# Optimization experiments

Measured on AMD Instinct MI355X. Metric: run time of the kernel, lower is better.

Reference implementation:

```python
import jax, jax.numpy as jnp
import numpy as np

T, B, D, H, R, O = 32, 8, 512, 512, 32, 512
CLIP_VAL = 1.0
LN_EPS = 1e-5


def setup_inputs() -> dict:
    key = jax.random.key(0)
    ks = jax.random.split(key, 8)
    rn = lambda k, sh, sc: (jax.random.normal(k, sh) * sc).astype(jnp.float32)
    inp = {
        'x': rn(ks[0], (T, B, D), 1.0),
        'h0': jnp.zeros((B, H), jnp.float32),
        'v0': jnp.zeros((B, H), jnp.float32),
        'dU0': jnp.zeros((B, H, H), jnp.float32),
        'trace_e0': jnp.zeros((B, H), jnp.float32),
        'trace_E0': jnp.zeros((B, H, H), jnp.float32),
        # parameters (init-scale approximations of the torch inits)
        'x2h_w': rn(ks[1], (2 * H, D), 1.0 / np.sqrt(D)),
        'x2h_b': jnp.zeros((2 * H,), jnp.float32),
        'h2h_w': rn(ks[2], (2 * H, H), 1.0 / np.sqrt(H)),
        'h2h_b': jnp.zeros((2 * H,), jnp.float32),
        'lnx_g': jnp.ones((2 * H,), jnp.float32),
        'lnx_b': jnp.zeros((2 * H,), jnp.float32),
        'lnh_g': jnp.ones((2 * H,), jnp.float32),
        'lnh_b': jnp.zeros((2 * H,), jnp.float32),
        'h2mod_w': rn(ks[3], (R, H), np.sqrt(2.0 / H)),
        'h2mod_b': jnp.zeros((R,), jnp.float32),
        'mod2h_w': rn(ks[4], (3, R), np.sqrt(2.0 / R)),
        'mod2h_b': jnp.zeros((3,), jnp.float32),
        'alpha': jnp.full((1,), -4.0, jnp.float32),
        'tau_U': jnp.full((1,), -4.5, jnp.float32),
        'dec_w': rn(ks[5], (O, H), 1.0 / np.sqrt(H)),
        'dec_b': jnp.zeros((O,), jnp.float32),
    }
    return inp


def _ln(y, g, b):
    mu = jnp.mean(y, axis=-1, keepdims=True)
    yc = y - mu
    var = jnp.mean(yc * yc, axis=-1, keepdims=True)
    return g * yc * jax.lax.rsqrt(var + LN_EPS) + b


def reference(x, h0, v0, dU0, trace_e0, trace_E0,
              x2h_w, x2h_b, h2h_w, h2h_b,
              lnx_g, lnx_b, lnh_g, lnh_b,
              h2mod_w, h2mod_b, mod2h_w, mod2h_b,
              alpha, tau_U, dec_w, dec_b):
    Hh = h0.shape[-1]
    sp_alpha = jax.nn.softplus(alpha)            # (1,)
    tau = jax.nn.sigmoid(tau_U)                  # (1,)
    # clip bounds derived from the candidate-row block of h2h weight
    w_dv = h2h_w[Hh:2 * Hh]                      # [H, H]
    upper = jax.nn.relu(CLIP_VAL - w_dv) / (sp_alpha + 1e-8)
    lower = -jax.nn.relu(CLIP_VAL + w_dv) / (sp_alpha + 1e-8)

    def step(carry, xt):
        h, v, dU, te, tE = carry
        Wx = _ln(xt @ x2h_w.T + x2h_b, lnx_g, lnx_b)           # [B, 2H]
        Wh = h @ h2h_w.T + h2h_b                               # [B, 2H]
        plast = sp_alpha * jnp.einsum('bij,bj->bi', dU, h)     # [B, H]
        Wh = Wh.at[:, Hh:].add(plast)
        Wh = _ln(Wh, lnh_g, lnh_b)
        z, dv = jnp.split(Wx + Wh, 2, axis=-1)
        z = jax.nn.sigmoid(z)
        v_n = (1.0 - z) * v + z * dv
        nh = jax.nn.relu(v_n)
        mod = jax.nn.relu(nh @ h2mod_w.T + h2mod_b) @ mod2h_w.T + mod2h_b  # [B, 3]
        r = jax.nn.sigmoid(mod[:, :1])                          # [B, 1]
        s = jax.nn.sigmoid(mod[:, 1])[:, None, None]            # [B, 1, 1]
        m = mod[:, 2][:, None, None]                            # [B, 1, 1]
        te_n = (1.0 - r) * te + r * h
        outer = nh[:, :, None] * te_n[:, None, :]               # [B, H, H]
        tE_n = (1.0 - s) * tE + s * (outer - jnp.swapaxes(outer, 1, 2))
        dU_n = (1.0 - tau) * dU + tau * m * tE_n
        dU_n = jnp.where(dU_n > upper, upper, dU_n)
        dU_n = jnp.where(dU_n < lower, lower, dU_n)
        return (nh, v_n, dU_n, te_n, tE_n), nh

    carry0 = (h0, v0, dU0, trace_e0, trace_E0)
    _, hs = jax.lax.scan(step, carry0, x)                        # hs: [T, B, H]
    out = hs @ dec_w.T + dec_b                                   # [T, B, O]
    return out
```

## Files before the change

### kernel.cpp

```cpp
#include <hip/hip_runtime.h>

#define TT 32
#define BB 8
#define DD 512
#define HH 512
#define RR 32
#define OO 512
#define H2 1024

typedef unsigned int uint;

#define OFF_WX    0
#define OFF_HS    262144
#define OFF_COLV  393216
#define OFF_FLAGS 409600

#define AGENT __HIP_MEMORY_SCOPE_AGENT
#define RLX   __ATOMIC_RELAXED

#define HMW_P 528

__device__ __forceinline__ void st_coh(float* p, float v) {
  __hip_atomic_store(p, v, RLX, AGENT);
}
__device__ __forceinline__ float ld_coh(const float* p) {
  return __hip_atomic_load(const_cast<float*>(p), RLX, AGENT);
}
__device__ __forceinline__ float d4(const float4& a, const float4& b) {
  return a.x*b.x + a.y*b.y + a.z*b.z + a.w*b.w;
}

__device__ __forceinline__ void bar32(unsigned* flags, int b, int ir,
                                      unsigned seq, int tid) {
  __syncthreads();
  asm volatile("s_waitcnt vmcnt(0)" ::: "memory");
  if (tid == 0)
    __hip_atomic_store(&flags[b*32 + ir], seq, RLX, AGENT);
  if (tid < 64) {
    for (;;) {
      unsigned v = (tid < 32) ? __hip_atomic_load(&flags[b*32 + tid], RLX, AGENT) : seq;
      if (__all(v >= seq)) break;
      __builtin_amdgcn_s_sleep(1);
    }
  }
  __syncthreads();
}

template<bool UPDATE>
__device__ __forceinline__ void gemv_step(
    int gi, int m,
    float4 (&dUr)[4], float4 (&tEr)[4],
    const float4 (&Wdvr)[4], const float4 (&wlo)[4],
    const float4 (&upr)[4], const float4 (&lor)[4],
    float s_b, float c1t, float c2t, float a_sp, float hbl, float hbh,
    const float* nh_s, const float* te_s,
    float* post)
{
  const float nh_i = nh_s[gi];
  const float te_i = UPDATE ? te_s[gi] : 0.0f;
  const float4* nh4 = reinterpret_cast<const float4*>(nh_s);
  const float4* te4 = reinterpret_cast<const float4*>(te_s);
  float plast = 0.0f, gdv = 0.0f, glo = 0.0f;
#pragma unroll
  for (int q = 0; q < 4; ++q) {
    const int J = m + 32*q;
    const float4 h4 = nh4[J];
    if (UPDATE) {
      const float4 t4 = te4[J];
#define SGRU_UPD(C) { \
      float o   = nh_i * t4.C - h4.C * te_i;                 \
      float tEn = tEr[q].C + s_b * (o - tEr[q].C);           \
      tEr[q].C  = tEn;                                                               \
      float d   = c1t * dUr[q].C + c2t * tEn;                \
      d = fminf(d, upr[q].C); d = fmaxf(d, lor[q].C);        \
      dUr[q].C  = d;                                                                 \
      plast = fmaf(d, h4.C, plast); }
      SGRU_UPD(x) SGRU_UPD(y) SGRU_UPD(z) SGRU_UPD(w)
#undef SGRU_UPD
    } else {
      plast += d4(dUr[q], h4);
    }
    gdv += d4(Wdvr[q], h4);
    glo += d4(wlo[q],  h4);
  }
#pragma unroll
  for (int off = 16; off >= 1; off >>= 1) {
    plast += __shfl_xor(plast, off);
    gdv   += __shfl_xor(gdv, off);
    glo   += __shfl_xor(glo, off);
  }
  if (m == 0) {
    st_coh(&post[gi],      glo + hbl);
    st_coh(&post[HH + gi], gdv + hbh + a_sp * plast);
  }
}

__global__ __launch_bounds__(512, 1) void sgru_persistent(
    const float* __restrict__ h0,     const float* __restrict__ v0,
    const float* __restrict__ dU0,    const float* __restrict__ tE0,
    const float* __restrict__ te0,
    const float* __restrict__ h2h_w,  const float* __restrict__ h2h_b,
    const float* __restrict__ lnh_g,  const float* __restrict__ lnh_b,
    const float* __restrict__ h2mod_w,const float* __restrict__ h2mod_b,
    const float* __restrict__ mod2h_w,const float* __restrict__ mod2h_b,
    const float* __restrict__ alpha_p,const float* __restrict__ tau_p,
    float* __restrict__ ws)
{
  const int tid = threadIdx.x;
  const int b   = blockIdx.x & 7;
  const int ir  = blockIdx.x >> 3;
  const int i0  = ir << 4;
  const int il  = tid >> 5;
  const int m   = tid & 31;
  const int gi  = i0 + il;

  const float* Wx = ws + OFF_WX;
  float* hsbuf    = ws + OFF_HS;
  float* colvG    = ws + OFF_COLV;
  unsigned* flags = (unsigned*)(ws + OFF_FLAGS);

  __shared__ float nh_s[2][HH];
  __shared__ float te_s[HH];
  __shared__ float hmw_s[RR * HMW_P];
  __shared__ float mp_s[RR];
  __shared__ float rsm_s[4];
  __shared__ float red_s[2][8];

  const float a_sp  = log1pf(__expf(alpha_p[0]));
  const float inv_a = 1.0f / (a_sp + 1e-8f);
  const float tau   = 1.0f / (1.0f + __expf(-tau_p[0]));
  const float c1t   = 1.0f - tau;

  float4 dUr[4], tEr[4], Wdvr[4], wlo[4], upr[4], lor[4];
  {
    const size_t rowoff = ((size_t)b * HH + gi) * HH;
    const size_t whioff = (size_t)(HH + gi) * HH;
    const size_t wlooff = (size_t)gi * HH;
#pragma unroll
    for (int q = 0; q < 4; ++q) {
      const int J = m + 32*q;
      dUr[q] = *reinterpret_cast<const float4*>(dU0 + rowoff + 4*J);
      tEr[q] = *reinterpret_cast<const float4*>(tE0 + rowoff + 4*J);
      wlo[q] = *reinterpret_cast<const float4*>(h2h_w + wlooff + 4*J);
      const float4 w = *reinterpret_cast<const float4*>(h2h_w + whioff + 4*J);
      Wdvr[q] = w;
      float4 u, l;
      u.x =  fmaxf(1.0f - w.x, 0.0f) * inv_a;  l.x = -fmaxf(1.0f + w.x, 0.0f) * inv_a;
      u.y =  fmaxf(1.0f - w.y, 0.0f) * inv_a;  l.y = -fmaxf(1.0f + w.y, 0.0f) * inv_a;
      u.z =  fmaxf(1.0f - w.z, 0.0f) * inv_a;  l.z = -fmaxf(1.0f + w.z, 0.0f) * inv_a;
      u.w =  fmaxf(1.0f - w.w, 0.0f) * inv_a;  l.w = -fmaxf(1.0f + w.w, 0.0f) * inv_a;
      upr[q] = u; lor[q] = l;
    }
  }

  const float rgz = lnh_g[tid],      rbz = lnh_b[tid];
  const float rgd = lnh_g[HH + tid], rbd = lnh_b[HH + tid];
  const float hbl = h2h_b[gi], hbh = h2h_b[HH + gi];
  const float hmb = h2mod_b[tid >> 4];
  const float mw0 = (tid < RR) ? mod2h_w[tid]        : 0.0f;
  const float mw1 = (tid < RR) ? mod2h_w[RR + tid]   : 0.0f;
  const float mw2 = (tid < RR) ? mod2h_w[2*RR + tid] : 0.0f;
  const float mb0 = mod2h_b[0], mb1 = mod2h_b[1], mb2 = mod2h_b[2];
  float vreg = v0[b*HH + tid];

  nh_s[1][tid] = h0[b*HH + tid];
  te_s[tid]    = te0[b*HH + tid];
  for (int idx = tid; idx < RR*HH; idx += 512)
    hmw_s[(idx >> 9)*HMW_P + (idx & 511)] = h2mod_w[idx];
  __syncthreads();

  gemv_step<false>(gi, m, dUr, tEr, Wdvr, wlo, upr, lor,
                   0.0f, c1t, 0.0f, a_sp, hbl, hbh,
                   nh_s[1], te_s, colvG + 0*BB*H2 + b*H2);

  float wxz = Wx[(size_t)(0*BB + b)*H2 + tid];
  float wxd = Wx[(size_t)(0*BB + b)*H2 + HH + tid];

  unsigned seq = 0;
  for (int t = 0; t < TT; ++t) {
    const int cur = t & 1;
    bar32(flags, b, ir, ++seq, tid);

    const float whz = ld_coh(&colvG[cur*BB*H2 + b*H2 + tid]);
    const float whd = ld_coh(&colvG[cur*BB*H2 + b*H2 + HH + tid]);

    float s1 = whz + whd, s2 = whz*whz + whd*whd;
#pragma unroll
    for (int off = 32; off >= 1; off >>= 1) {
      s1 += __shfl_xor(s1, off);
      s2 += __shfl_xor(s2, off);
    }
    if ((tid & 63) == 0) { red_s[0][tid >> 6] = s1; red_s[1][tid >> 6] = s2; }
    __syncthreads();
    s1 = 0.0f; s2 = 0.0f;
#pragma unroll
    for (int w = 0; w < 8; ++w) { s1 += red_s[0][w]; s2 += red_s[1][w]; }
    const float mu   = s1 * (1.0f / H2);
    const float var  = s2 * (1.0f / H2) - mu * mu;
    const float rstd = rsqrtf(var + 1e-5f);

    const float yz = (whz - mu)*rstd*rgz + rbz + wxz;
    const float yd = (whd - mu)*rstd*rgd + rbd + wxd;
    const float z  = 1.0f / (1.0f + __expf(-yz));
    vreg = vreg + z * (yd - vreg);
    const float nh = fmaxf(vreg, 0.0f);
    nh_s[cur][tid] = nh;
    if (ir == 0) hsbuf[(size_t)(t*BB + b)*HH + tid] = nh;
    if (t == TT - 1) return;

    wxz = Wx[(size_t)((t+1)*BB + b)*H2 + tid];
    wxd = Wx[(size_t)((t+1)*BB + b)*H2 + HH + tid];
    __syncthreads();

    {
      const int r = tid >> 4, kk = tid & 15;
      float part = 0.0f;
#pragma unroll
      for (int j = 0; j < 32; ++j)
        part += hmw_s[r*HMW_P + kk + 16*j] * nh_s[cur][kk + 16*j];
#pragma unroll
      for (int off = 8; off >= 1; off >>= 1) part += __shfl_xor(part, off);
      if (kk == 0) mp_s[r] = fmaxf(part + hmb, 0.0f);
    }
    __syncthreads();
    if (tid < 64) {
      const float mp = (tid < RR) ? mp_s[tid] : 0.0f;
      float a0 = mw0*mp, a1 = mw1*mp, a2 = mw2*mp;
#pragma unroll
      for (int off = 16; off >= 1; off >>= 1) {
        a0 += __shfl_xor(a0, off);
        a1 += __shfl_xor(a1, off);
        a2 += __shfl_xor(a2, off);
      }
      if (tid == 0) {
        rsm_s[0] = 1.0f / (1.0f + __expf(-(a0 + mb0)));
        rsm_s[1] = 1.0f / (1.0f + __expf(-(a1 + mb1)));
        rsm_s[2] = a2 + mb2;
      }
    }
    __syncthreads();
    const float r_b = rsm_s[0];
    const float s_b = rsm_s[1];
    const float c2t = tau * rsm_s[2];

    te_s[tid] += r_b * (nh_s[1 - cur][tid] - te_s[tid]);
    __syncthreads();

    gemv_step<true>(gi, m, dUr, tEr, Wdvr, wlo, upr, lor,
                    s_b, c1t, c2t, a_sp, hbl, hbh,
                    nh_s[cur], te_s, colvG + (1 - cur)*BB*H2 + b*H2);
  }
}

#define GBM 32
#define GBN 32
#define GBK 32
__global__ __launch_bounds__(256) void gemm_tn(
    const float* __restrict__ A, const float* __restrict__ W,
    const float* __restrict__ bias, float* __restrict__ C,
    int M, int N)
{
  const int K = 512;
  const int nbn = N / GBN;
  const int m0 = (blockIdx.x / nbn) * GBM;
  const int n0 = (blockIdx.x % nbn) * GBN;
  const int tid = threadIdx.x;
  const int tx = tid & 15;
  const int ty = tid >> 4;
  const int lr = tid >> 3;
  const int lc = tid & 7;
  __shared__ float As[GBK][36];
  __shared__ float Ws[GBK][36];
  float acc[2][2] = {};
  for (int kc = 0; kc < K; kc += GBK) {
    const float4 a0 = *reinterpret_cast<const float4*>(A + (size_t)(m0 + lr)*K + kc + lc*4);
    const float4 w0 = *reinterpret_cast<const float4*>(W + (size_t)(n0 + lr)*K + kc + lc*4);
    __syncthreads();
    As[lc*4+0][lr] = a0.x; As[lc*4+1][lr] = a0.y; As[lc*4+2][lr] = a0.z; As[lc*4+3][lr] = a0.w;
    Ws[lc*4+0][lr] = w0.x; Ws[lc*4+1][lr] = w0.y; Ws[lc*4+2][lr] = w0.z; Ws[lc*4+3][lr] = w0.w;
    __syncthreads();
#pragma unroll
    for (int k = 0; k < GBK; ++k) {
      const float2 am = *reinterpret_cast<const float2*>(&As[k][ty*2]);
      const float2 wn = *reinterpret_cast<const float2*>(&Ws[k][tx*2]);
      acc[0][0] += am.x*wn.x; acc[0][1] += am.x*wn.y;
      acc[1][0] += am.y*wn.x; acc[1][1] += am.y*wn.y;
    }
  }
  const float b0 = bias[n0 + tx*2], b1 = bias[n0 + tx*2 + 1];
  C[(size_t)(m0 + ty*2 + 0)*N + n0 + tx*2]     = acc[0][0] + b0;
  C[(size_t)(m0 + ty*2 + 0)*N + n0 + tx*2 + 1] = acc[0][1] + b1;
  C[(size_t)(m0 + ty*2 + 1)*N + n0 + tx*2]     = acc[1][0] + b0;
  C[(size_t)(m0 + ty*2 + 1)*N + n0 + tx*2 + 1] = acc[1][1] + b1;
}

__global__ __launch_bounds__(256) void ln_apply(
    float* __restrict__ Wp, const float* __restrict__ g, const float* __restrict__ b,
    unsigned* __restrict__ flags)
{
  const int row = blockIdx.x;
  const int tid = threadIdx.x;
  if (row == 0) flags[tid] = 0u;
  float* rp = Wp + (size_t)row * H2;
  float4 v = *reinterpret_cast<const float4*>(rp + tid*4);
  float s1 = v.x + v.y + v.z + v.w;
  float s2 = v.x*v.x + v.y*v.y + v.z*v.z + v.w*v.w;
#pragma unroll
  for (int off = 32; off >= 1; off >>= 1) {
    s1 += __shfl_xor(s1, off);
    s2 += __shfl_xor(s2, off);
  }
  __shared__ float red[2][4];
  if ((tid & 63) == 0) { red[0][tid >> 6] = s1; red[1][tid >> 6] = s2; }
  __syncthreads();
  s1 = red[0][0] + red[0][1] + red[0][2] + red[0][3];
  s2 = red[1][0] + red[1][1] + red[1][2] + red[1][3];
  const float mu   = s1 * (1.0f / H2);
  const float var  = s2 * (1.0f / H2) - mu * mu;
  const float rstd = rsqrtf(var + 1e-5f);
  const float4 gv = *reinterpret_cast<const float4*>(g + tid*4);
  const float4 bv = *reinterpret_cast<const float4*>(b + tid*4);
  v.x = gv.x*(v.x - mu)*rstd + bv.x;
  v.y = gv.y*(v.y - mu)*rstd + bv.y;
  v.z = gv.z*(v.z - mu)*rstd + bv.z;
  v.w = gv.w*(v.w - mu)*rstd + bv.w;
  *reinterpret_cast<float4*>(rp + tid*4) = v;
}

extern "C" void kernel_launch(void* const* d_in, const int* in_sizes, int n_in,
                              void* d_out, int out_size, void* d_ws, size_t ws_size,
                              hipStream_t stream) {
  (void)in_sizes; (void)n_in; (void)out_size; (void)ws_size;
  const float* x        = (const float*)d_in[0];
  const float* h0       = (const float*)d_in[1];
  const float* v0       = (const float*)d_in[2];
  const float* dU0      = (const float*)d_in[3];
  const float* te0      = (const float*)d_in[4];
  const float* tE0      = (const float*)d_in[5];
  const float* x2h_w    = (const float*)d_in[6];
  const float* x2h_b    = (const float*)d_in[7];
  const float* h2h_w    = (const float*)d_in[8];
  const float* h2h_b    = (const float*)d_in[9];
  const float* lnx_g    = (const float*)d_in[10];
  const float* lnx_b    = (const float*)d_in[11];
  const float* lnh_g    = (const float*)d_in[12];
  const float* lnh_b    = (const float*)d_in[13];
  const float* h2mod_w  = (const float*)d_in[14];
  const float* h2mod_b  = (const float*)d_in[15];
  const float* mod2h_w  = (const float*)d_in[16];
  const float* mod2h_b  = (const float*)d_in[17];
  const float* alpha    = (const float*)d_in[18];
  const float* tau_U    = (const float*)d_in[19];
  const float* dec_w    = (const float*)d_in[20];
  const float* dec_b    = (const float*)d_in[21];

  float* ws = (float*)d_ws;

  gemm_tn<<<(TT*BB/GBM) * (H2/GBN), 256, 0, stream>>>(x, x2h_w, x2h_b,
                                                      ws + OFF_WX, TT*BB, H2);
  ln_apply<<<TT*BB, 256, 0, stream>>>(ws + OFF_WX, lnx_g, lnx_b,
                                      (unsigned*)(ws + OFF_FLAGS));

  sgru_persistent<<<256, 512, 0, stream>>>(h0, v0, dU0, tE0, te0,
                                           h2h_w, h2h_b, lnh_g, lnh_b,
                                           h2mod_w, h2mod_b, mod2h_w, mod2h_b,
                                           alpha, tau_U, ws);

  gemm_tn<<<(TT*BB/GBM) * (OO/GBN), 256, 0, stream>>>(ws + OFF_HS, dec_w, dec_b,
                                                      (float*)d_out, TT*BB, OO);
}
```

Measured before the change: 174.7 us.

## Interleave two batches per block with split-phase flag barriers

Each persistent block now owns 8 rows for two batch elements (b and b+4) instead of 16 rows for one, and the kernel alternates phases between the two batches. While one batch waits on the cross-block barrier, the other batch's work can proceed, which is meant to hide synchronization latency. The barrier now signals arrival at the end of a phase and waits at the start of the next, polling the 64 flags of a group with 16-byte loads that use sc0/sc1 cache-bypass bits. The r/s/m modulation reduction is recomputed redundantly in every wave instead of going through shared memory with an extra __syncthreads. The cost is that each block holds register state for two batches and the flag array doubles in size.

```diff
diff --git a/kernel.cpp b/kernel.cpp
--- a/kernel.cpp
+++ b/kernel.cpp
@@ -9,6 +9,7 @@
 #define H2 1024
 
 typedef unsigned int uint;
+typedef uint u32x4 __attribute__((ext_vector_type(4)));
 
 #define OFF_WX    0
 #define OFF_HS    262144
@@ -26,46 +27,114 @@
 __device__ __forceinline__ float ld_coh(const float* p) {
   return __hip_atomic_load(const_cast<float*>(p), RLX, AGENT);
 }
+__device__ __forceinline__ u32x4 ld16_mall(const u32x4* p) {
+  u32x4 r;
+  asm volatile("global_load_dwordx4 %0, %1, off sc0 sc1\n\ts_waitcnt vmcnt(0)"
+               : "=v"(r) : "v"(p) : "memory");
+  return r;
+}
 __device__ __forceinline__ float d4(const float4& a, const float4& b) {
   return a.x*b.x + a.y*b.y + a.z*b.z + a.w*b.w;
 }
 
-__device__ __forceinline__ void bar32(unsigned* flags, int b, int ir,
-                                      unsigned seq, int tid) {
-  __syncthreads();
-  asm volatile("s_waitcnt vmcnt(0)" ::: "memory");
-  if (tid == 0)
-    __hip_atomic_store(&flags[b*32 + ir], seq, RLX, AGENT);
-  if (tid < 64) {
-    for (;;) {
-      unsigned v = (tid < 32) ? __hip_atomic_load(&flags[b*32 + tid], RLX, AGENT) : seq;
-      if (__all(v >= seq)) break;
-      __builtin_amdgcn_s_sleep(1);
-    }
-  }
-  __syncthreads();
-}
-
-template<bool UPDATE>
-__device__ __forceinline__ void gemv_step(
-    int gi, int m,
-    float4 (&dUr)[4], float4 (&tEr)[4],
-    const float4 (&Wdvr)[4], const float4 (&wlo)[4],
-    const float4 (&upr)[4], const float4 (&lor)[4],
-    float s_b, float c1t, float c2t, float a_sp, float hbl, float hbh,
-    const float* nh_s, const float* te_s,
-    float* post)
+template<bool LAST>
+__device__ __forceinline__ void phase(
+    int t, int cur, int b, int tid, int ir, int il, int m, int i0, int gi,
+    float4 (&dUr)[2], float4 (&tEr)[2], float& vreg, float& wxz, float& wxd,
+    const float4 (&wlo)[2], const float4 (&Wdvr)[2],
+    const float4 (&upr)[2], const float4 (&lor)[2],
+    float rgz, float rbz, float rgd, float rbd,
+    float hbl, float hbh, float hmb,
+    float mw0, float mw1, float mw2, float mb0, float mb1, float mb2,
+    float a_sp, float tau, float c1t,
+    float (*nh_s)[HH], float* te_s,
+    const float* hmw_s, float* mp_s, float (*red_s)[8],
+    const float* Wx, float* hsbuf, float* colvG, unsigned* flags)
 {
-  const float nh_i = nh_s[gi];
-  const float te_i = UPDATE ? te_s[gi] : 0.0f;
-  const float4* nh4 = reinterpret_cast<const float4*>(nh_s);
-  const float4* te4 = reinterpret_cast<const float4*>(te_s);
+  {
+    const uint want = (uint)(t + 1);
+    bool ok;
+    const u32x4* fp = (const u32x4*)(flags + b*64) + (tid & 15);
+    do {
+      u32x4 f = ld16_mall(fp);
+      ok = (tid < 64) ? ((f.x >= want) & (f.y >= want) & (f.z >= want) & (f.w >= want))
+                      : true;
+      if (tid < 64 && !ok) __builtin_amdgcn_s_sleep(1);
+    } while (tid < 64 && !ok);
+  }
+  __syncthreads();
+
+  const float whz = ld_coh(&colvG[cur*BB*H2 + b*H2 + tid]);
+  const float whd = ld_coh(&colvG[cur*BB*H2 + b*H2 + HH + tid]);
+
+  float s1 = whz + whd, s2 = whz*whz + whd*whd;
+#pragma unroll
+  for (int off = 32; off >= 1; off >>= 1) {
+    s1 += __shfl_xor(s1, off);
+    s2 += __shfl_xor(s2, off);
+  }
+  if ((tid & 63) == 0) { red_s[0][tid >> 6] = s1; red_s[1][tid >> 6] = s2; }
+  __syncthreads();
+  s1 = 0.0f; s2 = 0.0f;
+#pragma unroll
+  for (int w = 0; w < 8; ++w) { s1 += red_s[0][w]; s2 += red_s[1][w]; }
+  const float mu   = s1 * (1.0f / H2);
+  const float var  = s2 * (1.0f / H2) - mu * mu;
+  const float rstd = rsqrtf(var + 1e-5f);
+
+  const float yz = (whz - mu)*rstd*rgz + rbz + wxz;
+  const float yd = (whd - mu)*rstd*rgd + rbd + wxd;
+  const float z  = 1.0f / (1.0f + __expf(-yz));
+  vreg = vreg + z * (yd - vreg);
+  const float nh = fmaxf(vreg, 0.0f);
+  nh_s[cur][tid] = nh;
+  if (ir == 0) hsbuf[(size_t)(t*BB + b)*HH + tid] = nh;
+  if (LAST) return;
+
+  wxz = Wx[(size_t)((t+1)*BB + b)*H2 + tid];
+  wxd = Wx[(size_t)((t+1)*BB + b)*H2 + HH + tid];
+  __syncthreads();
+
+  {
+    const int r = tid >> 4, kk = tid & 15;
+    float part = 0.0f;
+#pragma unroll
+    for (int j = 0; j < 32; ++j)
+      part += hmw_s[r*HMW_P + kk + 16*j] * nh_s[cur][kk + 16*j];
+#pragma unroll
+    for (int off = 8; off >= 1; off >>= 1) part += __shfl_xor(part, off);
+    if (kk == 0) mp_s[r] = fmaxf(part + hmb, 0.0f);
+  }
+  __syncthreads();
+
+  float r_b, s_b, c2t;
+  {
+    const float mp = mp_s[tid & 31];
+    float a0 = mw0*mp, a1 = mw1*mp, a2 = mw2*mp;
+#pragma unroll
+    for (int off = 16; off >= 1; off >>= 1) {
+      a0 += __shfl_xor(a0, off);
+      a1 += __shfl_xor(a1, off);
+      a2 += __shfl_xor(a2, off);
+    }
+    r_b = 1.0f / (1.0f + __expf(-(a0 + mb0)));
+    s_b = 1.0f / (1.0f + __expf(-(a1 + mb1)));
+    c2t = tau * (a2 + mb2);
+  }
+
+  te_s[tid] += r_b * (nh_s[1 - cur][tid] - te_s[tid]);
+  __syncthreads();
+
+  const float nh_i = nh_s[cur][gi];
+  const float te_i = te_s[gi];
   float plast = 0.0f, gdv = 0.0f, glo = 0.0f;
-#pragma unroll
-  for (int q = 0; q < 4; ++q) {
-    const int J = m + 32*q;
-    const float4 h4 = nh4[J];
-    if (UPDATE) {
+  {
+    const float4* nh4 = reinterpret_cast<const float4*>(nh_s[cur]);
+    const float4* te4 = reinterpret_cast<const float4*>(te_s);
+#pragma unroll
+    for (int q = 0; q < 2; ++q) {
+      const int J = m + 64*q;
+      const float4 h4 = nh4[J];
       const float4 t4 = te4[J];
 #define SGRU_UPD(C) { \
       float o   = nh_i * t4.C - h4.C * te_i;                 \
@@ -77,22 +146,24 @@
       plast = fmaf(d, h4.C, plast); }
       SGRU_UPD(x) SGRU_UPD(y) SGRU_UPD(z) SGRU_UPD(w)
 #undef SGRU_UPD
-    } else {
-      plast += d4(dUr[q], h4);
-    }
-    gdv += d4(Wdvr[q], h4);
-    glo += d4(wlo[q],  h4);
-  }
-#pragma unroll
-  for (int off = 16; off >= 1; off >>= 1) {
-    plast += __shfl_xor(plast, off);
-    gdv   += __shfl_xor(gdv, off);
-    glo   += __shfl_xor(glo, off);
-  }
+      gdv += d4(Wdvr[q], h4);
+      glo += d4(wlo[q],  h4);
+    }
+#pragma unroll
+    for (int off = 32; off >= 1; off >>= 1) {
+      plast += __shfl_xor(plast, off);
+      gdv   += __shfl_xor(gdv, off);
+      glo   += __shfl_xor(glo, off);
+    }
+  }
+  float* post = colvG + (1 - cur)*BB*H2 + b*H2;
   if (m == 0) {
     st_coh(&post[gi],      glo + hbl);
     st_coh(&post[HH + gi], gdv + hbh + a_sp * plast);
   }
+  __syncthreads();
+  if (tid == 0)
+    __hip_atomic_store(&flags[b*64 + ir], (uint)(t + 2), RLX, AGENT);
 }
 
 __global__ __launch_bounds__(512, 1) void sgru_persistent(
@@ -107,11 +178,12 @@
     float* __restrict__ ws)
 {
   const int tid = threadIdx.x;
-  const int b   = blockIdx.x & 7;
-  const int ir  = blockIdx.x >> 3;
-  const int i0  = ir << 4;
-  const int il  = tid >> 5;
-  const int m   = tid & 31;
+  const int bg  = blockIdx.x & 3;
+  const int ir  = blockIdx.x >> 2;
+  const int bA  = bg, bB = bg + 4;
+  const int i0  = ir << 3;
+  const int il  = tid >> 6;
+  const int m   = tid & 63;
   const int gi  = i0 + il;
 
   const float* Wx = ws + OFF_WX;
@@ -119,11 +191,10 @@
   float* colvG    = ws + OFF_COLV;
   unsigned* flags = (unsigned*)(ws + OFF_FLAGS);
 
-  __shared__ float nh_s[2][HH];
-  __shared__ float te_s[HH];
+  __shared__ float nhA_s[2][HH], nhB_s[2][HH];
+  __shared__ float teA_s[HH], teB_s[HH];
   __shared__ float hmw_s[RR * HMW_P];
   __shared__ float mp_s[RR];
-  __shared__ float rsm_s[4];
   __shared__ float red_s[2][8];
 
   const float a_sp  = log1pf(__expf(alpha_p[0]));
@@ -131,16 +202,13 @@
   const float tau   = 1.0f / (1.0f + __expf(-tau_p[0]));
   const float c1t   = 1.0f - tau;
 
-  float4 dUr[4], tEr[4], Wdvr[4], wlo[4], upr[4], lor[4];
-  {
-    const size_t rowoff = ((size_t)b * HH + gi) * HH;
+  float4 wlo[2], Wdvr[2], upr[2], lor[2];
+  {
     const size_t whioff = (size_t)(HH + gi) * HH;
     const size_t wlooff = (size_t)gi * HH;
 #pragma unroll
-    for (int q = 0; q < 4; ++q) {
-      const int J = m + 32*q;
-      dUr[q] = *reinterpret_cast<const float4*>(dU0 + rowoff + 4*J);
-      tEr[q] = *reinterpret_cast<const float4*>(tE0 + rowoff + 4*J);
+    for (int q = 0; q < 2; ++q) {
+      const int J = m + 64*q;
       wlo[q] = *reinterpret_cast<const float4*>(h2h_w + wlooff + 4*J);
       const float4 w = *reinterpret_cast<const float4*>(h2h_w + whioff + 4*J);
       Wdvr[q] = w;
@@ -152,103 +220,100 @@
       upr[q] = u; lor[q] = l;
     }
   }
+  float4 dUrA[2], tErA[2], dUrB[2], tErB[2];
+  {
+    const size_t rowA = ((size_t)bA * HH + gi) * HH;
+    const size_t rowB = ((size_t)bB * HH + gi) * HH;
+#pragma unroll
+    for (int q = 0; q < 2; ++q) {
+      const int J = m + 64*q;
+      dUrA[q] = *reinterpret_cast<const float4*>(dU0 + rowA + 4*J);
+      tErA[q] = *reinterpret_cast<const float4*>(tE0 + rowA + 4*J);
+      dUrB[q] = *reinterpret_cast<const float4*>(dU0 + rowB + 4*J);
+      tErB[q] = *reinterpret_cast<const float4*>(tE0 + rowB + 4*J);
+    }
+  }
 
   const float rgz = lnh_g[tid],      rbz = lnh_b[tid];
   const float rgd = lnh_g[HH + tid], rbd = lnh_b[HH + tid];
   const float hbl = h2h_b[gi], hbh = h2h_b[HH + gi];
   const float hmb = h2mod_b[tid >> 4];
-  const float mw0 = (tid < RR) ? mod2h_w[tid]        : 0.0f;
-  const float mw1 = (tid < RR) ? mod2h_w[RR + tid]   : 0.0f;
-  const float mw2 = (tid < RR) ? mod2h_w[2*RR + tid] : 0.0f;
+  const float mw0 = mod2h_w[tid & 31];
+  const float mw1 = mod2h_w[RR + (tid & 31)];
+  const float mw2 = mod2h_w[2*RR + (tid & 31)];
   const float mb0 = mod2h_b[0], mb1 = mod2h_b[1], mb2 = mod2h_b[2];
-  float vreg = v0[b*HH + tid];
-
-  nh_s[1][tid] = h0[b*HH + tid];
-  te_s[tid]    = te0[b*HH + tid];
+  float vregA = v0[bA*HH + tid];
+  float vregB = v0[bB*HH + tid];
+
+  nhA_s[1][tid] = h0[bA*HH + tid];
+  nhB_s[1][tid] = h0[bB*HH + tid];
+  teA_s[tid]    = te0[bA*HH + tid];
+  teB_s[tid]    = te0[bB*HH + tid];
   for (int idx = tid; idx < RR*HH; idx += 512)
     hmw_s[(idx >> 9)*HMW_P + (idx & 511)] = h2mod_w[idx];
   __syncthreads();
 
-  gemv_step<false>(gi, m, dUr, tEr, Wdvr, wlo, upr, lor,
-                   0.0f, c1t, 0.0f, a_sp, hbl, hbh,
-                   nh_s[1], te_s, colvG + 0*BB*H2 + b*H2);
-
-  float wxz = Wx[(size_t)(0*BB + b)*H2 + tid];
-  float wxd = Wx[(size_t)(0*BB + b)*H2 + HH + tid];
-
-  unsigned seq = 0;
-  for (int t = 0; t < TT; ++t) {
+  {
+    const float4* hA4 = reinterpret_cast<const float4*>(nhA_s[1]);
+    const float4* hB4 = reinterpret_cast<const float4*>(nhB_s[1]);
+    float gloA = 0.0f, gdvA = 0.0f, plA = 0.0f;
+    float gloB = 0.0f, gdvB = 0.0f, plB = 0.0f;
+#pragma unroll
+    for (int q = 0; q < 2; ++q) {
+      const int J = m + 64*q;
+      const float4 a4 = hA4[J], b4 = hB4[J];
+      gloA += d4(wlo[q], a4);  gdvA += d4(Wdvr[q], a4);  plA += d4(dUrA[q], a4);
+      gloB += d4(wlo[q], b4);  gdvB += d4(Wdvr[q], b4);  plB += d4(dUrB[q], b4);
+    }
+#pragma unroll
+    for (int off = 32; off >= 1; off >>= 1) {
+      gloA += __shfl_xor(gloA, off); gdvA += __shfl_xor(gdvA, off); plA += __shfl_xor(plA, off);
+      gloB += __shfl_xor(gloB, off); gdvB += __shfl_xor(gdvB, off); plB += __shfl_xor(plB, off);
+    }
+    if (m == 0) {
+      st_coh(&colvG[0*BB*H2 + bA*H2 + gi],      gloA + hbl);
+      st_coh(&colvG[0*BB*H2 + bA*H2 + HH + gi], gdvA + hbh + a_sp*plA);
+      st_coh(&colvG[0*BB*H2 + bB*H2 + gi],      gloB + hbl);
+      st_coh(&colvG[0*BB*H2 + bB*H2 + HH + gi], gdvB + hbh + a_sp*plB);
+    }
+    __syncthreads();
+    if (tid == 0) {
+      __hip_atomic_store(&flags[bA*64 + ir], 1u, RLX, AGENT);
+      __hip_atomic_store(&flags[bB*64 + ir], 1u, RLX, AGENT);
+    }
+  }
+
+  float wxzA = Wx[(size_t)(0*BB + bA)*H2 + tid];
+  float wxdA = Wx[(size_t)(0*BB + bA)*H2 + HH + tid];
+  float wxzB = Wx[(size_t)(0*BB + bB)*H2 + tid];
+  float wxdB = Wx[(size_t)(0*BB + bB)*H2 + HH + tid];
+
+#pragma unroll 1
+  for (int t = 0; t < TT - 1; ++t) {
     const int cur = t & 1;
-    bar32(flags, b, ir, ++seq, tid);
-
-    const float whz = ld_coh(&colvG[cur*BB*H2 + b*H2 + tid]);
-    const float whd = ld_coh(&colvG[cur*BB*H2 + b*H2 + HH + tid]);
-
-    float s1 = whz + whd, s2 = whz*whz + whd*whd;
-#pragma unroll
-    for (int off = 32; off >= 1; off >>= 1) {
-      s1 += __shfl_xor(s1, off);
-      s2 += __shfl_xor(s2, off);
-    }
-    if ((tid & 63) == 0) { red_s[0][tid >> 6] = s1; red_s[1][tid >> 6] = s2; }
-    __syncthreads();
-    s1 = 0.0f; s2 = 0.0f;
-#pragma unroll
-    for (int w = 0; w < 8; ++w) { s1 += red_s[0][w]; s2 += red_s[1][w]; }
-    const float mu   = s1 * (1.0f / H2);
-    const float var  = s2 * (1.0f / H2) - mu * mu;
-    const float rstd = rsqrtf(var + 1e-5f);
-
-    const float yz = (whz - mu)*rstd*rgz + rbz + wxz;
-    const float yd = (whd - mu)*rstd*rgd + rbd + wxd;
-    const float z  = 1.0f / (1.0f + __expf(-yz));
-    vreg = vreg + z * (yd - vreg);
-    const float nh = fmaxf(vreg, 0.0f);
-    nh_s[cur][tid] = nh;
-    if (ir == 0) hsbuf[(size_t)(t*BB + b)*HH + tid] = nh;
-    if (t == TT - 1) return;
-
-    wxz = Wx[(size_t)((t+1)*BB + b)*H2 + tid];
-    wxd = Wx[(size_t)((t+1)*BB + b)*H2 + HH + tid];
-    __syncthreads();
-
-    {
-      const int r = tid >> 4, kk = tid & 15;
-      float part = 0.0f;
-#pragma unroll
-      for (int j = 0; j < 32; ++j)
-        part += hmw_s[r*HMW_P + kk + 16*j] * nh_s[cur][kk + 16*j];
-#pragma unroll
-      for (int off = 8; off >= 1; off >>= 1) part += __shfl_xor(part, off);
-      if (kk == 0) mp_s[r] = fmaxf(part + hmb, 0.0f);
-    }
-    __syncthreads();
-    if (tid < 64) {
-      const float mp = (tid < RR) ? mp_s[tid] : 0.0f;
-      float a0 = mw0*mp, a1 = mw1*mp, a2 = mw2*mp;
-#pragma unroll
-      for (int off = 16; off >= 1; off >>= 1) {
-        a0 += __shfl_xor(a0, off);
-        a1 += __shfl_xor(a1, off);
-        a2 += __shfl_xor(a2, off);
-      }
-      if (tid == 0) {
-        rsm_s[0] = 1.0f / (1.0f + __expf(-(a0 + mb0)));
-        rsm_s[1] = 1.0f / (1.0f + __expf(-(a1 + mb1)));
-        rsm_s[2] = a2 + mb2;
-      }
-    }
-    __syncthreads();
-    const float r_b = rsm_s[0];
-    const float s_b = rsm_s[1];
-    const float c2t = tau * rsm_s[2];
-
-    te_s[tid] += r_b * (nh_s[1 - cur][tid] - te_s[tid]);
-    __syncthreads();
-
-    gemv_step<true>(gi, m, dUr, tEr, Wdvr, wlo, upr, lor,
-                    s_b, c1t, c2t, a_sp, hbl, hbh,
-                    nh_s[cur], te_s, colvG + (1 - cur)*BB*H2 + b*H2);
+    phase<false>(t, cur, bA, tid, ir, il, m, i0, gi,
+                 dUrA, tErA, vregA, wxzA, wxdA, wlo, Wdvr, upr, lor,
+                 rgz, rbz, rgd, rbd, hbl, hbh, hmb,
+                 mw0, mw1, mw2, mb0, mb1, mb2, a_sp, tau, c1t,
+                 nhA_s, teA_s, hmw_s, mp_s, red_s, Wx, hsbuf, colvG, flags);
+    phase<false>(t, cur, bB, tid, ir, il, m, i0, gi,
+                 dUrB, tErB, vregB, wxzB, wxdB, wlo, Wdvr, upr, lor,
+                 rgz, rbz, rgd, rbd, hbl, hbh, hmb,
+                 mw0, mw1, mw2, mb0, mb1, mb2, a_sp, tau, c1t,
+                 nhB_s, teB_s, hmw_s, mp_s, red_s, Wx, hsbuf, colvG, flags);
+  }
+  {
+    const int t = TT - 1, cur = t & 1;
+    phase<true>(t, cur, bA, tid, ir, il, m, i0, gi,
+                dUrA, tErA, vregA, wxzA, wxdA, wlo, Wdvr, upr, lor,
+                rgz, rbz, rgd, rbd, hbl, hbh, hmb,
+                mw0, mw1, mw2, mb0, mb1, mb2, a_sp, tau, c1t,
+                nhA_s, teA_s, hmw_s, mp_s, red_s, Wx, hsbuf, colvG, flags);
+    phase<true>(t, cur, bB, tid, ir, il, m, i0, gi,
+                dUrB, tErB, vregB, wxzB, wxdB, wlo, Wdvr, upr, lor,
+                rgz, rbz, rgd, rbd, hbl, hbh, hmb,
+                mw0, mw1, mw2, mb0, mb1, mb2, a_sp, tau, c1t,
+                nhB_s, teB_s, hmw_s, mp_s, red_s, Wx, hsbuf, colvG, flags);
   }
 }
 
@@ -300,7 +365,10 @@
 {
   const int row = blockIdx.x;
   const int tid = threadIdx.x;
-  if (row == 0) flags[tid] = 0u;
+  if (row == 0) {
+    flags[tid]       = 0u;
+    flags[tid + 256] = 0u;
+  }
   float* rp = Wp + (size_t)row * H2;
   float4 v = *reinterpret_cast<const float4*>(rp + tid*4);
   float s1 = v.x + v.y + v.z + v.w;
```

Measured after the change: 254.4 us. +45.6%, slower.

## Fuse decoder projection into persistent recurrent kernel, drop final GEMM launch

Applied to the files above, without the earlier changes.

Each block computes its 16 output rows of the decoder projection for its batch at every timestep, using the nh vector already held in shared memory. This removes the hs workspace buffer and the separate output GEMM launch. The cost is extra per-step work inside the latency-bound recurrent loop: dec_w rows are reloaded from global memory every step and a warp reduction is added, which could lengthen the critical path.

```diff
diff --git a/kernel.cpp b/kernel.cpp
--- a/kernel.cpp
+++ b/kernel.cpp
@@ -11,7 +11,6 @@
 typedef unsigned int uint;
 
 #define OFF_WX    0
-#define OFF_HS    262144
 #define OFF_COLV  393216
 #define OFF_FLAGS 409600
 
@@ -104,7 +103,8 @@
     const float* __restrict__ h2mod_w,const float* __restrict__ h2mod_b,
     const float* __restrict__ mod2h_w,const float* __restrict__ mod2h_b,
     const float* __restrict__ alpha_p,const float* __restrict__ tau_p,
-    float* __restrict__ ws)
+    const float* __restrict__ dec_w,  const float* __restrict__ dec_b,
+    float* __restrict__ out,          float* __restrict__ ws)
 {
   const int tid = threadIdx.x;
   const int b   = blockIdx.x & 7;
@@ -115,7 +115,6 @@
   const int gi  = i0 + il;
 
   const float* Wx = ws + OFF_WX;
-  float* hsbuf    = ws + OFF_HS;
   float* colvG    = ws + OFF_COLV;
   unsigned* flags = (unsigned*)(ws + OFF_FLAGS);
 
@@ -161,6 +160,8 @@
   const float mw1 = (tid < RR) ? mod2h_w[RR + tid]   : 0.0f;
   const float mw2 = (tid < RR) ? mod2h_w[2*RR + tid] : 0.0f;
   const float mb0 = mod2h_b[0], mb1 = mod2h_b[1], mb2 = mod2h_b[2];
+  const float dbc = dec_b[gi];
+  const float* drow = dec_w + (size_t)gi * HH;
   float vreg = v0[b*HH + tid];
 
   nh_s[1][tid] = h0[b*HH + tid];
@@ -205,8 +206,21 @@
     vreg = vreg + z * (yd - vreg);
     const float nh = fmaxf(vreg, 0.0f);
     nh_s[cur][tid] = nh;
-    if (ir == 0) hsbuf[(size_t)(t*BB + b)*HH + tid] = nh;
-    if (t == TT - 1) return;
+
+    if (t == TT - 1) {
+      __syncthreads();
+      const float4* nh4 = reinterpret_cast<const float4*>(nh_s[cur]);
+      float acc = 0.0f;
+#pragma unroll
+      for (int q = 0; q < 4; ++q) {
+        const int J = m + 32*q;
+        acc += d4(*reinterpret_cast<const float4*>(drow + 4*J), nh4[J]);
+      }
+#pragma unroll
+      for (int off = 16; off >= 1; off >>= 1) acc += __shfl_xor(acc, off);
+      if (m == 0) out[(size_t)(t*BB + b)*OO + gi] = acc + dbc;
+      return;
+    }
 
     wxz = Wx[(size_t)((t+1)*BB + b)*H2 + tid];
     wxd = Wx[(size_t)((t+1)*BB + b)*H2 + HH + tid];
@@ -249,6 +263,19 @@
     gemv_step<true>(gi, m, dUr, tEr, Wdvr, wlo, upr, lor,
                     s_b, c1t, c2t, a_sp, hbl, hbh,
                     nh_s[cur], te_s, colvG + (1 - cur)*BB*H2 + b*H2);
+
+    {
+      const float4* nh4 = reinterpret_cast<const float4*>(nh_s[cur]);
+      float acc = 0.0f;
+#pragma unroll
+      for (int q = 0; q < 4; ++q) {
+        const int J = m + 32*q;
+        acc += d4(*reinterpret_cast<const float4*>(drow + 4*J), nh4[J]);
+      }
+#pragma unroll
+      for (int off = 16; off >= 1; off >>= 1) acc += __shfl_xor(acc, off);
+      if (m == 0) out[(size_t)(t*BB + b)*OO + gi] = acc + dbc;
+    }
   }
 }
 
@@ -364,8 +391,6 @@
   sgru_persistent<<<256, 512, 0, stream>>>(h0, v0, dU0, tE0, te0,
                                            h2h_w, h2h_b, lnh_g, lnh_b,
                                            h2mod_w, h2mod_b, mod2h_w, mod2h_b,
-                                           alpha, tau_U, ws);
-
-  gemm_tn<<<(TT*BB/GBM) * (OO/GBN), 256, 0, stream>>>(ws + OFF_HS, dec_w, dec_b,
-                                                      (float*)d_out, TT*BB, OO);
-}
+                                           alpha, tau_U, dec_w, dec_b,
+                                           (float*)d_out, ws);
+}
```

Measured after the change: 177.3 us. About the same (+1.5%).
